# Optimization experiments

Hardware: AMD Instinct MI355X
Metric: run time of the kernel (lower is better)

Reference implementation:

```python
import jax, jax.numpy as jnp
import numpy as np

# Grid config: nuScenes-style BEV grid
XMIN, XMAX, DX = -51.2, 51.2, 0.4
YMIN, YMAX, DY = -51.2, 51.2, 0.4
ZMIN, ZMAX, DZ = -5.0, 3.0, 8.0
NX = int((XMAX - XMIN) / DX)  # 256
NY = int((YMAX - YMIN) / DY)  # 256
NZ = int((ZMAX - ZMIN) / DZ)  # 1
B, N, F = 8, 500000, 18       # batch, points per cloud, radar_feat_dim


def setup_inputs() -> dict:
    key = jax.random.key(0)
    pts = jax.random.normal(key, (B, N, F), dtype=jnp.float32)
    # spread xyz across the [-51.2, 51.2] grid (some points fall outside -> masked)
    pts = pts.at[..., :3].multiply(20.0)
    return {"points": pts}


def reference(points):
    """Scatter-mean rasterization of radar points into a dense BEV grid.

    points: (B, N, 18) float32. Returns (B, F*NZ, NY, NX).
    Equivalent math to the torch running-mean scatter: per-voxel mean of the
    18-dim features of all in-range points falling into that voxel.
    """
    x, y, z = points[..., 0], points[..., 1], points[..., 2]
    mask = ((x >= XMIN) & (x <= XMAX) &
            (y >= YMIN) & (y <= YMAX) &
            (z >= ZMIN) & (z <= ZMAX))
    sx, sy, sz = NX / (XMAX - XMIN), NY / (YMAX - YMIN), NZ / (ZMAX - ZMIN)
    ix = jnp.clip(((x - XMIN) * sx).astype(jnp.int32), 0, NX - 1)
    iy = jnp.clip(((y - YMIN) * sy).astype(jnp.int32), 0, NY - 1)
    iz = jnp.clip(((z - ZMIN) * sz).astype(jnp.int32), 0, NZ - 1)
    # global linear voxel index, batch-offset so one segment_sum covers all B
    lin = (iz * (NY * NX) + iy * NX + ix
           + jnp.arange(B, dtype=jnp.int32)[:, None] * (NZ * NY * NX))
    lin = lin.reshape(-1)                              # (B*N,)
    w = mask.astype(points.dtype).reshape(-1)          # (B*N,) 0/1 weights
    feats = points.reshape(-1, F) * w[:, None]         # masked-out -> 0 contribution
    nseg = B * NZ * NY * NX
    sums = jax.ops.segment_sum(feats, lin, num_segments=nseg)  # (nseg, F)
    cnts = jax.ops.segment_sum(w, lin, num_segments=nseg)      # (nseg,)
    mean = sums / jnp.maximum(cnts, 1.0)[:, None]
    grid = mean.reshape(B, NZ, NY, NX, F)
    grid = jnp.transpose(grid, (0, 4, 1, 2, 3))        # (B, F, NZ, NY, NX)
    return grid.reshape(B, F * NZ, NY, NX)
```

## Files before the change

### kernel.cpp

```cpp
#include <hip/hip_runtime.h>


#define B_     8
#define NPTS   500000
#define F_     18
#define NX_    256
#define NY_    256
#define NVOX   (NX_ * NY_)
#define BN     (B_ * NPTS)
#define NVOXT  (B_ * NVOX)
#define CAP    32

typedef float float4u __attribute__((ext_vector_type(4), aligned(4)));
typedef float float2u __attribute__((ext_vector_type(2), aligned(4)));

__global__ __launch_bounds__(256) void bin_kernel(const float* __restrict__ pts,
                                                  unsigned* __restrict__ cnt,
                                                  unsigned* __restrict__ list) {
    int p = blockIdx.x * 256 + threadIdx.x;
    float4u a = *(const float4u*)(pts + (size_t)p * F_);
    float x = a.x, y = a.y, z = a.z;
    bool ok = (x >= -51.2f) & (x <= 51.2f) &
              (y >= -51.2f) & (y <= 51.2f) &
              (z >= -5.0f)  & (z <= 3.0f);
    if (!ok) return;

    int ix = min(max((int)((x + 51.2f) * 2.5f), 0), NX_ - 1);
    int iy = min(max((int)((y + 51.2f) * 2.5f), 0), NY_ - 1);
    int b  = p / NPTS;
    int vox = b * NVOX + iy * NX_ + ix;

    unsigned slot = atomicAdd(cnt + vox, 1u);
    if (slot < CAP) list[(size_t)slot * NVOXT + vox] = (unsigned)p;
}

__global__ __launch_bounds__(256) void reduce_kernel(const float* __restrict__ pts,
                                                     const unsigned* __restrict__ cnt,
                                                     const unsigned* __restrict__ list,
                                                     float* __restrict__ out) {
    int t = blockIdx.x * 256 + threadIdx.x;
    int v = t >> 2;
    int k = t & 3;
    int b   = v >> 16;
    int pos = v & (NVOX - 1);

    unsigned c = min(cnt[v], (unsigned)CAP);

    float s[F_];
#pragma unroll
    for (int f = 0; f < F_; ++f) s[f] = 0.0f;

    for (unsigned i = k; i < c; i += 4) {
        unsigned p = list[(size_t)i * NVOXT + v];
        const float* rec = pts + (size_t)p * F_;
        float4u w0 = ((const float4u*)rec)[0];
        float4u w1 = ((const float4u*)rec)[1];
        float4u w2 = ((const float4u*)rec)[2];
        float4u w3 = ((const float4u*)rec)[3];
        float2u w4 = *(const float2u*)(rec + 16);
        s[0]  += w0.x; s[1]  += w0.y; s[2]  += w0.z; s[3]  += w0.w;
        s[4]  += w1.x; s[5]  += w1.y; s[6]  += w1.z; s[7]  += w1.w;
        s[8]  += w2.x; s[9]  += w2.y; s[10] += w2.z; s[11] += w2.w;
        s[12] += w3.x; s[13] += w3.y; s[14] += w3.z; s[15] += w3.w;
        s[16] += w4.x; s[17] += w4.y;
    }

#pragma unroll
    for (int f = 0; f < F_; ++f) {
        s[f] += __shfl_xor(s[f], 1);
        s[f] += __shfl_xor(s[f], 2);
    }

    if (k == 0) {
        float rcp = (c > 0) ? (1.0f / (float)c) : 0.0f;
        float* ob = out + (((size_t)b * F_) << 16) + pos;
#pragma unroll
        for (int f = 0; f < F_; ++f) ob[(size_t)f << 16] = s[f] * rcp;
    }
}

extern "C" void kernel_launch(void* const* d_in, const int* in_sizes, int n_in,
                              void* d_out, int out_size, void* d_ws, size_t ws_size,
                              hipStream_t stream) {
    const float* pts = (const float*)d_in[0];
    float* out = (float*)d_out;
    unsigned* cnt  = (unsigned*)d_ws;
    unsigned* list = cnt + NVOXT;

    hipMemsetAsync(cnt, 0, (size_t)NVOXT * sizeof(unsigned), stream);

    bin_kernel<<<BN / 256, 256, 0, stream>>>(pts, cnt, list);
    reduce_kernel<<<(NVOXT * 4) / 256, 256, 0, stream>>>(pts, cnt, list, out);
}
```

Before: 424.0 us.

## Compact in-range point records during binning for contiguous reduce gathers

The binning pass now copies each in-range point into a compact, 16-byte-aligned 80-byte record buffer. Slots are allocated with one wave-level ballot and atomic per partition, and the voxel lists store these compact indices instead of original point indices. The reduce pass gathers from the smaller, aligned compact buffer instead of scattered 72-byte records across the full input. The aim is to shrink the gather working set so more of it stays in cache, and to allow aligned vector loads. In exchange, binning does extra writes, partition atomics and a larger workspace.

```diff
diff --git a/kernel.cpp b/kernel.cpp
--- a/kernel.cpp
+++ b/kernel.cpp
@@ -10,20 +10,54 @@
 #define BN     (B_ * NPTS)
 #define NVOXT  (B_ * NVOX)
 #define CAP    32
+#define RSTRIDE 20
+#define NPART  64
+#define CAPREC 65536
 
 typedef float float4u __attribute__((ext_vector_type(4), aligned(4)));
 typedef float float2u __attribute__((ext_vector_type(2), aligned(4)));
 
 __global__ __launch_bounds__(256) void bin_kernel(const float* __restrict__ pts,
                                                   unsigned* __restrict__ cnt,
-                                                  unsigned* __restrict__ list) {
-    int p = blockIdx.x * 256 + threadIdx.x;
-    float4u a = *(const float4u*)(pts + (size_t)p * F_);
+                                                  unsigned* __restrict__ list,
+                                                  float* __restrict__ compact,
+                                                  unsigned* __restrict__ gcount) {
+    const int tid = threadIdx.x;
+    const int p = blockIdx.x * 256 + tid;
+    const float* rec = pts + (size_t)p * F_;
+    float4u a = *(const float4u*)rec;
     float x = a.x, y = a.y, z = a.z;
     bool ok = (x >= -51.2f) & (x <= 51.2f) &
               (y >= -51.2f) & (y <= 51.2f) &
               (z >= -5.0f)  & (z <= 3.0f);
+
+    unsigned long long m = __ballot(ok);
     if (!ok) return;
+
+    const int lane = tid & 63;
+    const int w    = tid >> 6;
+    const int leader = (int)__ffsll((unsigned long long)m) - 1;
+    unsigned nact = (unsigned)__popcll(m);
+    unsigned rank = (unsigned)__popcll(m & ((1ull << lane) - 1ull));
+    const int part = (blockIdx.x * 4 + w) & (NPART - 1);
+
+    unsigned base;
+    if (lane == leader)
+        base = atomicAdd(gcount + part * 16, nact);
+    base = __shfl(base, leader);
+
+    unsigned cid = (unsigned)part * CAPREC + base + rank;
+
+    float4u t1 = ((const float4u*)rec)[1];
+    float4u t2 = ((const float4u*)rec)[2];
+    float4u t3 = ((const float4u*)rec)[3];
+    float2u t4 = *(const float2u*)(rec + 16);
+    float4* dst = (float4*)(compact + (size_t)cid * RSTRIDE);
+    dst[0] = make_float4(a.x,  a.y,  a.z,  a.w);
+    dst[1] = make_float4(t1.x, t1.y, t1.z, t1.w);
+    dst[2] = make_float4(t2.x, t2.y, t2.z, t2.w);
+    dst[3] = make_float4(t3.x, t3.y, t3.z, t3.w);
+    dst[4] = make_float4(t4.x, t4.y, 0.0f, 0.0f);
 
     int ix = min(max((int)((x + 51.2f) * 2.5f), 0), NX_ - 1);
     int iy = min(max((int)((y + 51.2f) * 2.5f), 0), NY_ - 1);
@@ -31,12 +65,12 @@
     int vox = b * NVOX + iy * NX_ + ix;
 
     unsigned slot = atomicAdd(cnt + vox, 1u);
-    if (slot < CAP) list[(size_t)slot * NVOXT + vox] = (unsigned)p;
+    if (slot < CAP) list[(size_t)slot * NVOXT + vox] = cid;
 }
 
-__global__ __launch_bounds__(256) void reduce_kernel(const float* __restrict__ pts,
-                                                     const unsigned* __restrict__ cnt,
+__global__ __launch_bounds__(256) void reduce_kernel(const unsigned* __restrict__ cnt,
                                                      const unsigned* __restrict__ list,
+                                                     const float* __restrict__ compact,
                                                      float* __restrict__ out) {
     int t = blockIdx.x * 256 + threadIdx.x;
     int v = t >> 2;
@@ -51,13 +85,9 @@
     for (int f = 0; f < F_; ++f) s[f] = 0.0f;
 
     for (unsigned i = k; i < c; i += 4) {
-        unsigned p = list[(size_t)i * NVOXT + v];
-        const float* rec = pts + (size_t)p * F_;
-        float4u w0 = ((const float4u*)rec)[0];
-        float4u w1 = ((const float4u*)rec)[1];
-        float4u w2 = ((const float4u*)rec)[2];
-        float4u w3 = ((const float4u*)rec)[3];
-        float2u w4 = *(const float2u*)(rec + 16);
+        unsigned cid = list[(size_t)i * NVOXT + v];
+        const float4* rp = (const float4*)(compact + (size_t)cid * RSTRIDE);
+        float4 w0 = rp[0], w1 = rp[1], w2 = rp[2], w3 = rp[3], w4 = rp[4];
         s[0]  += w0.x; s[1]  += w0.y; s[2]  += w0.z; s[3]  += w0.w;
         s[4]  += w1.x; s[5]  += w1.y; s[6]  += w1.z; s[7]  += w1.w;
         s[8]  += w2.x; s[9]  += w2.y; s[10] += w2.z; s[11] += w2.w;
@@ -84,11 +114,13 @@
                               hipStream_t stream) {
     const float* pts = (const float*)d_in[0];
     float* out = (float*)d_out;
-    unsigned* cnt  = (unsigned*)d_ws;
-    unsigned* list = cnt + NVOXT;
+    float* compact  = (float*)d_ws;
+    unsigned* list  = (unsigned*)(compact + (size_t)NPART * CAPREC * RSTRIDE);
+    unsigned* cnt   = list + (size_t)CAP * NVOXT;
+    unsigned* gcount = cnt + NVOXT;
 
-    hipMemsetAsync(cnt, 0, (size_t)NVOXT * sizeof(unsigned), stream);
+    hipMemsetAsync(cnt, 0, (size_t)(NVOXT + NPART * 16) * sizeof(unsigned), stream);
 
-    bin_kernel<<<BN / 256, 256, 0, stream>>>(pts, cnt, list);
-    reduce_kernel<<<(NVOXT * 4) / 256, 256, 0, stream>>>(pts, cnt, list, out);
+    bin_kernel<<<BN / 256, 256, 0, stream>>>(pts, cnt, list, compact, gcount);
+    reduce_kernel<<<(NVOXT * 4) / 256, 256, 0, stream>>>(cnt, list, compact, out);
 }
```

New measurement: 437.2 us. +3.1%, slower.
